# Kernel tuning notes

Measured on AMD Instinct MI355X. Metric: run time of the kernel, lower is better.

The kernel has to match this reference:

```python
import jax, jax.numpy as jnp
import numpy as np

N_GRAPHS = 128   # number of graphs in the batch
G = 128          # nodes per graph (equal-sized ragged blocks for the reference)
D = 512          # node embedding dim (feature_dim)
EPS = 1e-7


def setup_inputs() -> dict:
    key = jax.random.key(0)
    embeddings = jax.random.normal(key, (N_GRAPHS * G, D), dtype=jnp.float32)
    # Precompute block-diagonal strict-upper-triangular mask as gather indices.
    # Equivalent to torch.block_diag(*[triu(ones(g,g), diagonal=1) for g in sizes]).bool()
    iu_r, iu_c = np.triu_indices(G, k=1)                 # per-block triu(.,1) indices
    offsets = (np.arange(N_GRAPHS) * G)[:, None]         # block offsets into [N, N]
    row_idx = jnp.asarray((offsets + iu_r[None, :]).ravel(), dtype=jnp.int32)
    col_idx = jnp.asarray((offsets + iu_c[None, :]).ravel(), dtype=jnp.int32)
    return {"embeddings": embeddings, "row_idx": row_idx, "col_idx": col_idx}


def reference(embeddings, row_idx, col_idx):
    # Full NxN dot-product similarity (N = total nodes across all graphs).
    sims = embeddings @ embeddings.T                     # [N, N]
    m = sims.min()
    M = sims.max()
    sims = (sims - m) / (M - m + EPS)                    # global min-max normalization
    # Gather block-diagonal strict-upper-triangular entries -> flat vector.
    return sims[row_idx, col_idx]                        # [sum_g g*(g-1)/2]
```

## Files before the change

kernel.cpp:

```cpp
#include <hip/hip_runtime.h>
#include <hip/hip_bf16.h>
#include <stdint.h>


typedef __attribute__((ext_vector_type(8))) __bf16 bf16x8;
typedef __attribute__((ext_vector_type(16))) float floatx16;
typedef __attribute__((ext_vector_type(4))) int intx4;
typedef __attribute__((ext_vector_type(16))) int intx16;

#define AS1 __attribute__((address_space(1)))
#define AS3 __attribute__((address_space(3)))

static constexpr int DIM      = 512;
static constexpr int NTILE    = 128;
static constexpr int GX       = 72;
static constexpr int NPAIRIDX = 65 * 128;
static constexpr float QS     = 19.5f;
static constexpr int MARGIN_I = 3042;


static __device__ __forceinline__ unsigned short f2bf_rne(float f) {
  unsigned int u = __float_as_uint(f);
  u += 0x7fffu + ((u >> 16) & 1u);
  return (unsigned short)(u >> 16);
}
static __device__ __forceinline__ int fkey(float f) {
  int s = __float_as_int(f);
  return s >= 0 ? s : (s ^ 0x7fffffff);
}
static __device__ __forceinline__ float funkey(int k) {
  return __int_as_float(k >= 0 ? k : (k ^ 0x7fffffff));
}
static __device__ __forceinline__ int swzd(int row, int c16) {
  return c16 ^ (row & 15);
}
static __device__ __forceinline__ int swz8(int row, int c8) {
  return c8 ^ (row & 7);
}
static __device__ __forceinline__ int qswap(int v) {
  return (v & 0x7A) | ((v & 1) << 2) | ((v >> 2) & 1);
}
static __device__ __forceinline__ int sfun(int row) {
  return (row & 3) ^ ((row >> 3) & 3);
}

__global__ void k_convert(const float* __restrict__ in,
                          unsigned short* __restrict__ bf,
                          char* __restrict__ q,
                          int* __restrict__ ctrl, int n4) {
  int i = blockIdx.x * blockDim.x + threadIdx.x;
  if (i == 0) {
    ctrl[0] = 0x7fffffff; ctrl[1] = (int)0x80000000;
    ctrl[2] = 0x7fffffff;
  }
  if (i >= n4) return;
  float4 v = ((const float4*)in)[i];
  ushort4 o;
  o.x = f2bf_rne(v.x); o.y = f2bf_rne(v.y);
  o.z = f2bf_rne(v.z); o.w = f2bf_rne(v.w);
  ((ushort4*)bf)[i] = o;
  int qx = __float2int_rn(v.x * QS), qy = __float2int_rn(v.y * QS);
  int qz = __float2int_rn(v.z * QS), qw = __float2int_rn(v.w * QS);
  char4 c;
  c.x = (char)min(127, max(-127, qx));
  c.y = (char)min(127, max(-127, qy));
  c.z = (char)min(127, max(-127, qz));
  c.w = (char)min(127, max(-127, qw));
  ((char4*)q)[i] = c;
}

__global__ __launch_bounds__(512, 4) void k_gemm(
    const char* __restrict__ Eq,
    const unsigned short* __restrict__ E,
    int* __restrict__ ipart,
    float* __restrict__ diagblocks,
    int* __restrict__ ctrl) {
  const int x  = blockIdx.x;
  const int tr = blockIdx.y;
  if (x > 64) return;
  const int pi = tr * 65 + x;

  const int tid = threadIdx.x;
  __shared__ __align__(16) char smem[2][24576];
  __shared__ float2 redbuf[8];
  __shared__ int iredbuf[8];

  const int w = tid >> 6, lane = tid & 63;
  const int l31 = lane & 31;
  const int kg  = lane >> 5;

  if (x < 64) {
    const int tc1 = 2 * x + 1;
    if (tc1 <= tr) {
      if (tid == 0) ipart[pi] = 0x7fffffff;
      return;
    }
    const int tc0 = (2 * x > tr) ? 2 * x : tc1;

    const int rowA  = tr  * 128;
    const int rowB0 = tc0 * 128;
    const int rowB1 = tc1 * 128;

    const int wr = w >> 2;
    const int wcq = w & 3;
    const int bplane = 8192 + (wcq >> 1) * 8192;

    intx16 acc[2][2];
#pragma unroll
    for (int i = 0; i < 2; i++)
#pragma unroll
      for (int j = 0; j < 2; j++)
#pragma unroll
        for (int r = 0; r < 16; r++) acc[i][j][r] = 0;

#define STAGE3(bb, kt) do {                                                   \
    int p_   = tid;                                                           \
    int q_   = p_ >> 2;                                                       \
    int row_ = qswap(q_);                                                     \
    int off_ = (kt) * 64 + (((p_ & 3) ^ sfun(row_)) * 16);                    \
    char* d_ = smem[bb] + p_ * 16;                                            \
    __builtin_amdgcn_global_load_lds(                                         \
        (const AS1 unsigned int*)(Eq + (size_t)(rowA + row_) * DIM + off_),   \
        (AS3 unsigned int*)d_, 16, 0, 0);                                     \
    __builtin_amdgcn_global_load_lds(                                         \
        (const AS1 unsigned int*)(Eq + (size_t)(rowB0 + row_) * DIM + off_),  \
        (AS3 unsigned int*)(d_ + 8192), 16, 0, 0);                            \
    __builtin_amdgcn_global_load_lds(                                         \
        (const AS1 unsigned int*)(Eq + (size_t)(rowB1 + row_) * DIM + off_),  \
        (AS3 unsigned int*)(d_ + 16384), 16, 0, 0);                           \
  } while (0)

    const int ra0 = wr * 64 + l31,        ra1 = wr * 64 + 32 + l31;
    const int rb0 = (wcq & 1) * 64 + l31, rb1 = (wcq & 1) * 64 + 32 + l31;
    const int pa0 = qswap(ra0) * 64, sa0 = sfun(ra0);
    const int pa1 = qswap(ra1) * 64, sa1 = sfun(ra1);
    const int pb0 = qswap(rb0) * 64, sb0 = sfun(rb0);
    const int pb1 = qswap(rb1) * 64, sb1 = sfun(rb1);

    STAGE3(0, 0);
    __syncthreads();

#pragma unroll
    for (int kt = 0; kt < 8; kt++) {
      if (kt + 1 < 8) STAGE3((kt + 1) & 1, kt + 1);
      const char* cb = smem[kt & 1];
#pragma unroll
      for (int ks = 0; ks < 2; ks++) {
        const int c = ks * 2 + kg;
        intx4 af0 = *(const intx4*)(cb +           pa0 + ((c ^ sa0) << 4));
        intx4 af1 = *(const intx4*)(cb +           pa1 + ((c ^ sa1) << 4));
        intx4 bf0 = *(const intx4*)(cb + bplane +  pb0 + ((c ^ sb0) << 4));
        intx4 bf1 = *(const intx4*)(cb + bplane +  pb1 + ((c ^ sb1) << 4));
        acc[0][0] = __builtin_amdgcn_mfma_i32_32x32x32_i8(af0, bf0, acc[0][0], 0, 0, 0);
        acc[0][1] = __builtin_amdgcn_mfma_i32_32x32x32_i8(af0, bf1, acc[0][1], 0, 0, 0);
        acc[1][0] = __builtin_amdgcn_mfma_i32_32x32x32_i8(af1, bf0, acc[1][0], 0, 0, 0);
        acc[1][1] = __builtin_amdgcn_mfma_i32_32x32x32_i8(af1, bf1, acc[1][1], 0, 0, 0);
      }
      __syncthreads();
    }
#undef STAGE3

    int vmin = 0x7fffffff;
#pragma unroll
    for (int ti = 0; ti < 2; ti++)
#pragma unroll
      for (int tj = 0; tj < 2; tj++)
#pragma unroll
        for (int r = 0; r < 16; r++) vmin = min(vmin, acc[ti][tj][r]);
#pragma unroll
    for (int m_ = 32; m_ >= 1; m_ >>= 1)
      vmin = min(vmin, __shfl_xor(vmin, m_));
    if (lane == 0) iredbuf[w] = vmin;
    __syncthreads();
    if (tid == 0) {
      int mn = iredbuf[0];
      for (int i = 1; i < 8; i++) mn = min(mn, iredbuf[i]);
      ipart[pi] = mn;
      atomicMin(&ctrl[2], mn);
    }
  } else {
    if (tid == 0) ipart[pi] = 0x7fffffff;
    unsigned short* lA = (unsigned short*)&smem[0][0];
    const int wr = w >> 2, wcq = w & 3;
    floatx16 acc[2];
#pragma unroll
    for (int t = 0; t < 2; t++)
#pragma unroll
      for (int r = 0; r < 16; r++) acc[t][r] = 0.f;

    const int rowBase = tr * 128;

    for (int kb = 0; kb < 4; kb++) {
      const int kBase = kb * 128;
#pragma unroll
      for (int j = 0; j < 4; j++) {
        int p   = j * 512 + tid;
        int row = p >> 4, c16 = p & 15;
        int sc = swzd(row, c16);
        const unsigned short* gA =
            E + (size_t)(rowBase + row) * DIM + kBase + sc * 8;
        __builtin_amdgcn_global_load_lds((const AS1 unsigned int*)gA,
                                         (AS3 unsigned int*)(lA + p * 8), 16, 0, 0);
      }
      __syncthreads();

#pragma unroll
      for (int ks = 0; ks < 8; ks++) {
        bf16x8 af[2], bfv;
        const int c16 = ks * 2 + kg;
#pragma unroll
        for (int t = 0; t < 2; t++) {
          int ra = wr * 64 + t * 32 + l31;
          af[t]  = *(const bf16x8*)(lA + ra * 128 + swzd(ra, c16) * 8);
        }
        {
          int rb = wcq * 32 + l31;
          bfv = *(const bf16x8*)(lA + rb * 128 + swzd(rb, c16) * 8);
        }
#pragma unroll
        for (int t = 0; t < 2; t++)
          acc[t] = __builtin_amdgcn_mfma_f32_32x32x16_bf16(
              af[t], bfv, acc[t], 0, 0, 0);
      }
      __syncthreads();
    }

    float vmin = 3.4e38f, vmax = -3.4e38f;
#pragma unroll
    for (int t = 0; t < 2; t++)
#pragma unroll
      for (int r = 0; r < 16; r++) {
        float v = acc[t][r];
        vmin = fminf(vmin, v);
        vmax = fmaxf(vmax, v);
      }
#pragma unroll
    for (int m_ = 32; m_ >= 1; m_ >>= 1) {
      vmin = fminf(vmin, __shfl_xor(vmin, m_));
      vmax = fmaxf(vmax, __shfl_xor(vmax, m_));
    }
    if (lane == 0) redbuf[w] = make_float2(vmin, vmax);
    __syncthreads();
    if (tid == 0) {
      float mn = redbuf[0].x, mx = redbuf[0].y;
      for (int i = 1; i < 8; i++) {
        mn = fminf(mn, redbuf[i].x);
        mx = fmaxf(mx, redbuf[i].y);
      }
      atomicMin(&ctrl[0], fkey(mn));
      atomicMax(&ctrl[1], fkey(mx));
    }

    float* Bout = diagblocks + (size_t)tr * (128 * 128);
    const int cbase = wcq * 32 + l31;
#pragma unroll
    for (int t = 0; t < 2; t++) {
#pragma unroll
      for (int r = 0; r < 16; r++) {
        int row = wr * 64 + t * 32 + (r & 3) + 8 * (r >> 2) + 4 * kg;
        Bout[row * 128 + cbase] = acc[t][r];
      }
    }
  }
}

__global__ __launch_bounds__(256) void k_refine(
    const unsigned short* __restrict__ E,
    const int* __restrict__ ipart, int* __restrict__ ctrl) {
  const int pi = blockIdx.x;
  if (ipart[pi] > ctrl[2] + MARGIN_I) return;
  const int tr = pi / 65, x = pi % 65;
  if (x == 64) return;

  const int tid = threadIdx.x;
  __shared__ __align__(16) unsigned short lA[128 * 64];
  __shared__ __align__(16) unsigned short lB[128 * 64];
  __shared__ float redbuf[4];

  const int w = tid >> 6, lane = tid & 63;
  const int wr = w >> 1, wc = w & 1;
  const int l31 = lane & 31;
  const int kg  = lane >> 5;

  for (int s = 0; s < 2; s++) {
    const int tc = 2 * x + s;
    if (tc <= tr) continue;

    floatx16 acc[2][2];
#pragma unroll
    for (int i = 0; i < 2; i++)
#pragma unroll
      for (int j = 0; j < 2; j++)
#pragma unroll
        for (int r = 0; r < 16; r++) acc[i][j][r] = 0.f;

    const int rowBaseA = tr * 128;
    const int rowBaseB = tc * 128;

    for (int kb = 0; kb < 8; kb++) {
      const int kBase = kb * 64;
#pragma unroll
      for (int j = 0; j < 4; j++) {
        int cb  = (w * 4 + j) * 64;
        int p   = cb + lane;
        int row = p >> 3, c8 = p & 7;
        int sc8 = swz8(row, c8);
        const unsigned short* gA = E + (size_t)(rowBaseA + row) * DIM + kBase + sc8 * 8;
        const unsigned short* gB = E + (size_t)(rowBaseB + row) * DIM + kBase + sc8 * 8;
        __builtin_amdgcn_global_load_lds((const AS1 unsigned int*)gA,
                                         (AS3 unsigned int*)(lA + cb * 8), 16, 0, 0);
        __builtin_amdgcn_global_load_lds((const AS1 unsigned int*)gB,
                                         (AS3 unsigned int*)(lB + cb * 8), 16, 0, 0);
      }
      __syncthreads();

#pragma unroll
      for (int ks = 0; ks < 4; ks++) {
        bf16x8 af[2], bfv[2];
        const int c8 = ks * 2 + kg;
#pragma unroll
        for (int t = 0; t < 2; t++) {
          int ra = wr * 64 + t * 32 + l31;
          int rb = wc * 64 + t * 32 + l31;
          af[t]  = *(const bf16x8*)(lA + (ra * 8 + swz8(ra, c8)) * 8);
          bfv[t] = *(const bf16x8*)(lB + (rb * 8 + swz8(rb, c8)) * 8);
        }
#pragma unroll
        for (int ti = 0; ti < 2; ti++)
#pragma unroll
          for (int tj = 0; tj < 2; tj++)
            acc[ti][tj] = __builtin_amdgcn_mfma_f32_32x32x16_bf16(
                af[ti], bfv[tj], acc[ti][tj], 0, 0, 0);
      }
      __syncthreads();
    }

    float vmin = 3.4e38f;
#pragma unroll
    for (int ti = 0; ti < 2; ti++)
#pragma unroll
      for (int tj = 0; tj < 2; tj++)
#pragma unroll
        for (int r = 0; r < 16; r++) vmin = fminf(vmin, acc[ti][tj][r]);
#pragma unroll
    for (int m_ = 32; m_ >= 1; m_ >>= 1)
      vmin = fminf(vmin, __shfl_xor(vmin, m_));
    if (lane == 0) redbuf[w] = vmin;
    __syncthreads();
    if (tid == 0) {
      float mn = redbuf[0];
      for (int i = 1; i < 4; i++) mn = fminf(mn, redbuf[i]);
      atomicMin(&ctrl[0], fkey(mn));
    }
    __syncthreads();
  }
}

__global__ __launch_bounds__(256) void k_gather(
    const int* __restrict__ rix, const int* __restrict__ cix,
    const float* __restrict__ blocks, const int* __restrict__ ctrl,
    float* __restrict__ out, int n) {
  int i = blockIdx.x * blockDim.x + threadIdx.x;
  if (i >= n) return;
  float m   = funkey(ctrl[0]);
  float M   = funkey(ctrl[1]);
  float inv = 1.0f / (M - m + 1e-7f);
  int r = rix[i], c = cix[i];
  int g = r >> 7;
  float v = blocks[((size_t)g << 14) + ((r & 127) << 7) + (c & 127)];
  out[i] = (v - m) * inv;
}

extern "C" void kernel_launch(void* const* d_in, const int* in_sizes, int n_in,
                              void* d_out, int out_size, void* d_ws, size_t ws_size,
                              hipStream_t stream) {
  const float* emb = (const float*)d_in[0];
  const int* rix   = (const int*)d_in[1];
  const int* cix   = (const int*)d_in[2];

  char* ws = (char*)d_ws;
  int* ctrl           = (int*)ws;
  unsigned short* Ebf = (unsigned short*)(ws + 256);
  char* Eq            = (char*)(ws + 256 + (16u << 20));
  float* diagblocks   = (float*)(ws + 256 + (24u << 20));
  int* ipart          = (int*)(ws + 256 + (32u << 20));

  int n4 = in_sizes[0] / 4;

  k_convert<<<(n4 + 255) / 256, 256, 0, stream>>>(emb, Ebf, Eq, ctrl, n4);

  k_gemm<<<dim3(GX, 128), 512, 0, stream>>>(Eq, Ebf, ipart, diagblocks, ctrl);

  k_refine<<<NPAIRIDX, 256, 0, stream>>>(Ebf, ipart, ctrl);

  k_gather<<<(out_size + 255) / 256, 256, 0, stream>>>(rix, cix, diagblocks,
                                                       ctrl, (float*)d_out,
                                                       out_size);
}
```

Before: 191.4 us.

## Use 256x256 int8 GEMM tiles with cyclic tile-pair scheduling for min search

Enlarges the int8 min-search GEMM tile from 128x256 to 256x256 per workgroup. The upper-triangular pair enumeration becomes a cyclic (y + x) mod 64 schedule, which gives each workgroup the same amount of work. The refine kernel and the diagonal-block work are remapped to the new slot layout. The aim is better operand reuse per LDS load and no wasted or idle blocks from the triangular mask, at the cost of doubled LDS, more accumulator registers and lower occupancy. Since 33 cyclic offsets cover some tile pairs twice, it also does some redundant compute.

```diff
diff --git a/kernel.cpp b/kernel.cpp
--- a/kernel.cpp
+++ b/kernel.cpp
@@ -12,9 +12,8 @@
 #define AS3 __attribute__((address_space(3)))
 
 static constexpr int DIM      = 512;
-static constexpr int NTILE    = 128;
-static constexpr int GX       = 72;
-static constexpr int NPAIRIDX = 65 * 128;
+static constexpr int SLOTX    = 40;
+static constexpr int NSLOT    = SLOTX * 64;
 static constexpr float QS     = 19.5f;
 static constexpr int MARGIN_I = 3042;
 
@@ -69,19 +68,19 @@
   ((char4*)q)[i] = c;
 }
 
-__global__ __launch_bounds__(512, 4) void k_gemm(
+__global__ __launch_bounds__(512, 2) void k_gemm(
     const char* __restrict__ Eq,
     const unsigned short* __restrict__ E,
     int* __restrict__ ipart,
     float* __restrict__ diagblocks,
     int* __restrict__ ctrl) {
-  const int x  = blockIdx.x;
-  const int tr = blockIdx.y;
-  if (x > 64) return;
-  const int pi = tr * 65 + x;
+  const int x = blockIdx.x;
+  const int y = blockIdx.y;
+  if (x > 34) return;
+  const int pi = y * SLOTX + x;
 
   const int tid = threadIdx.x;
-  __shared__ __align__(16) char smem[2][24576];
+  __shared__ __align__(16) char smem[2][32768];
   __shared__ float2 redbuf[8];
   __shared__ int iredbuf[8];
 
@@ -89,82 +88,85 @@
   const int l31 = lane & 31;
   const int kg  = lane >> 5;
 
-  if (x < 64) {
-    const int tc1 = 2 * x + 1;
-    if (tc1 <= tr) {
-      if (tid == 0) ipart[pi] = 0x7fffffff;
-      return;
-    }
-    const int tc0 = (2 * x > tr) ? 2 * x : tc1;
-
-    const int rowA  = tr  * 128;
-    const int rowB0 = tc0 * 128;
-    const int rowB1 = tc1 * 128;
-
-    const int wr = w >> 2;
-    const int wcq = w & 3;
-    const int bplane = 8192 + (wcq >> 1) * 8192;
-
-    intx16 acc[2][2];
+  if (x < 33) {
+    const int tt = (y + x) & 63;
+    const int rA0 = 256 * y,  rA1 = 256 * y + 128;
+    const int rB0 = 256 * tt, rB1 = 256 * tt + 128;
+
+    const int wr = w >> 1, wc = w & 1;
+
+    intx16 acc[2][4];
 #pragma unroll
     for (int i = 0; i < 2; i++)
 #pragma unroll
-      for (int j = 0; j < 2; j++)
+      for (int j = 0; j < 4; j++)
 #pragma unroll
         for (int r = 0; r < 16; r++) acc[i][j][r] = 0;
 
-#define STAGE3(bb, kt) do {                                                   \
-    int p_   = tid;                                                           \
-    int q_   = p_ >> 2;                                                       \
+#define STAGE4(bb, kt) do {                                                   \
+    int q_   = tid >> 2;                                                      \
     int row_ = qswap(q_);                                                     \
-    int off_ = (kt) * 64 + (((p_ & 3) ^ sfun(row_)) * 16);                    \
-    char* d_ = smem[bb] + p_ * 16;                                            \
+    int off_ = (kt) * 64 + (((tid & 3) ^ sfun(row_)) * 16);                   \
+    char* d_ = smem[bb] + tid * 16;                                           \
     __builtin_amdgcn_global_load_lds(                                         \
-        (const AS1 unsigned int*)(Eq + (size_t)(rowA + row_) * DIM + off_),   \
+        (const AS1 unsigned int*)(Eq + (size_t)(rA0 + row_) * DIM + off_),    \
         (AS3 unsigned int*)d_, 16, 0, 0);                                     \
     __builtin_amdgcn_global_load_lds(                                         \
-        (const AS1 unsigned int*)(Eq + (size_t)(rowB0 + row_) * DIM + off_),  \
+        (const AS1 unsigned int*)(Eq + (size_t)(rA1 + row_) * DIM + off_),    \
         (AS3 unsigned int*)(d_ + 8192), 16, 0, 0);                            \
     __builtin_amdgcn_global_load_lds(                                         \
-        (const AS1 unsigned int*)(Eq + (size_t)(rowB1 + row_) * DIM + off_),  \
+        (const AS1 unsigned int*)(Eq + (size_t)(rB0 + row_) * DIM + off_),    \
         (AS3 unsigned int*)(d_ + 16384), 16, 0, 0);                           \
+    __builtin_amdgcn_global_load_lds(                                         \
+        (const AS1 unsigned int*)(Eq + (size_t)(rB1 + row_) * DIM + off_),    \
+        (AS3 unsigned int*)(d_ + 24576), 16, 0, 0);                           \
   } while (0)
 
-    const int ra0 = wr * 64 + l31,        ra1 = wr * 64 + 32 + l31;
-    const int rb0 = (wcq & 1) * 64 + l31, rb1 = (wcq & 1) * 64 + 32 + l31;
-    const int pa0 = qswap(ra0) * 64, sa0 = sfun(ra0);
-    const int pa1 = qswap(ra1) * 64, sa1 = sfun(ra1);
-    const int pb0 = qswap(rb0) * 64, sb0 = sfun(rb0);
-    const int pb1 = qswap(rb1) * 64, sb1 = sfun(rb1);
-
-    STAGE3(0, 0);
+    const int ra0 = wr * 64 + l31, ra1 = wr * 64 + 32 + l31;
+    const int pa0 = (ra0 >> 7) * 8192 + qswap(ra0 & 127) * 64, sa0 = sfun(ra0 & 127);
+    const int pa1 = (ra1 >> 7) * 8192 + qswap(ra1 & 127) * 64, sa1 = sfun(ra1 & 127);
+    const int rb0 = 0 * 32 + l31, rb1 = 1 * 32 + l31;
+    const int rb2 = 2 * 32 + l31, rb3 = 3 * 32 + l31;
+    const int pbB = 16384 + wc * 8192;
+    const int pb0 = pbB + qswap(rb0) * 64, sb0 = sfun(rb0);
+    const int pb1 = pbB + qswap(rb1) * 64, sb1 = sfun(rb1);
+    const int pb2 = pbB + qswap(rb2) * 64, sb2 = sfun(rb2);
+    const int pb3 = pbB + qswap(rb3) * 64, sb3 = sfun(rb3);
+
+    STAGE4(0, 0);
     __syncthreads();
 
 #pragma unroll
     for (int kt = 0; kt < 8; kt++) {
-      if (kt + 1 < 8) STAGE3((kt + 1) & 1, kt + 1);
+      if (kt + 1 < 8) STAGE4((kt + 1) & 1, kt + 1);
       const char* cb = smem[kt & 1];
 #pragma unroll
       for (int ks = 0; ks < 2; ks++) {
         const int c = ks * 2 + kg;
-        intx4 af0 = *(const intx4*)(cb +           pa0 + ((c ^ sa0) << 4));
-        intx4 af1 = *(const intx4*)(cb +           pa1 + ((c ^ sa1) << 4));
-        intx4 bf0 = *(const intx4*)(cb + bplane +  pb0 + ((c ^ sb0) << 4));
-        intx4 bf1 = *(const intx4*)(cb + bplane +  pb1 + ((c ^ sb1) << 4));
-        acc[0][0] = __builtin_amdgcn_mfma_i32_32x32x32_i8(af0, bf0, acc[0][0], 0, 0, 0);
-        acc[0][1] = __builtin_amdgcn_mfma_i32_32x32x32_i8(af0, bf1, acc[0][1], 0, 0, 0);
-        acc[1][0] = __builtin_amdgcn_mfma_i32_32x32x32_i8(af1, bf0, acc[1][0], 0, 0, 0);
-        acc[1][1] = __builtin_amdgcn_mfma_i32_32x32x32_i8(af1, bf1, acc[1][1], 0, 0, 0);
-      }
-      __syncthreads();
-    }
-#undef STAGE3
+        intx4 af0 = *(const intx4*)(cb + pa0 + ((c ^ sa0) << 4));
+        intx4 af1 = *(const intx4*)(cb + pa1 + ((c ^ sa1) << 4));
+        intx4 b0  = *(const intx4*)(cb + pb0 + ((c ^ sb0) << 4));
+        intx4 b1  = *(const intx4*)(cb + pb1 + ((c ^ sb1) << 4));
+        intx4 b2  = *(const intx4*)(cb + pb2 + ((c ^ sb2) << 4));
+        intx4 b3  = *(const intx4*)(cb + pb3 + ((c ^ sb3) << 4));
+        acc[0][0] = __builtin_amdgcn_mfma_i32_32x32x32_i8(af0, b0, acc[0][0], 0, 0, 0);
+        acc[0][1] = __builtin_amdgcn_mfma_i32_32x32x32_i8(af0, b1, acc[0][1], 0, 0, 0);
+        acc[0][2] = __builtin_amdgcn_mfma_i32_32x32x32_i8(af0, b2, acc[0][2], 0, 0, 0);
+        acc[0][3] = __builtin_amdgcn_mfma_i32_32x32x32_i8(af0, b3, acc[0][3], 0, 0, 0);
+        acc[1][0] = __builtin_amdgcn_mfma_i32_32x32x32_i8(af1, b0, acc[1][0], 0, 0, 0);
+        acc[1][1] = __builtin_amdgcn_mfma_i32_32x32x32_i8(af1, b1, acc[1][1], 0, 0, 0);
+        acc[1][2] = __builtin_amdgcn_mfma_i32_32x32x32_i8(af1, b2, acc[1][2], 0, 0, 0);
+        acc[1][3] = __builtin_amdgcn_mfma_i32_32x32x32_i8(af1, b3, acc[1][3], 0, 0, 0);
+      }
+      __syncthreads();
+    }
+#undef STAGE4
 
     int vmin = 0x7fffffff;
 #pragma unroll
     for (int ti = 0; ti < 2; ti++)
 #pragma unroll
-      for (int tj = 0; tj < 2; tj++)
+      for (int tj = 0; tj < 4; tj++)
 #pragma unroll
         for (int r = 0; r < 16; r++) vmin = min(vmin, acc[ti][tj][r]);
 #pragma unroll
@@ -180,6 +182,7 @@
     }
   } else {
     if (tid == 0) ipart[pi] = 0x7fffffff;
+    const int tr = 2 * y + (x - 33);
     unsigned short* lA = (unsigned short*)&smem[0][0];
     const int wr = w >> 2, wcq = w & 3;
     floatx16 acc[2];
@@ -269,8 +272,9 @@
     const int* __restrict__ ipart, int* __restrict__ ctrl) {
   const int pi = blockIdx.x;
   if (ipart[pi] > ctrl[2] + MARGIN_I) return;
-  const int tr = pi / 65, x = pi % 65;
-  if (x == 64) return;
+  const int y = pi / SLOTX, x = pi % SLOTX;
+  if (x >= 33) return;
+  const int tt = (y + x) & 63;
 
   const int tid = threadIdx.x;
   __shared__ __align__(16) unsigned short lA[128 * 64];
@@ -282,9 +286,9 @@
   const int l31 = lane & 31;
   const int kg  = lane >> 5;
 
-  for (int s = 0; s < 2; s++) {
-    const int tc = 2 * x + s;
-    if (tc <= tr) continue;
+  for (int ab = 0; ab < 4; ab++) {
+    const int rowBaseA = (2 * y + (ab >> 1)) * 128;
+    const int rowBaseB = (2 * tt + (ab & 1)) * 128;
 
     floatx16 acc[2][2];
 #pragma unroll
@@ -293,9 +297,6 @@
       for (int j = 0; j < 2; j++)
 #pragma unroll
         for (int r = 0; r < 16; r++) acc[i][j][r] = 0.f;
-
-    const int rowBaseA = tr * 128;
-    const int rowBaseB = tc * 128;
 
     for (int kb = 0; kb < 8; kb++) {
       const int kBase = kb * 64;
@@ -384,14 +385,13 @@
   char* Eq            = (char*)(ws + 256 + (16u << 20));
   float* diagblocks   = (float*)(ws + 256 + (24u << 20));
   int* ipart          = (int*)(ws + 256 + (32u << 20));
-
   int n4 = in_sizes[0] / 4;
 
   k_convert<<<(n4 + 255) / 256, 256, 0, stream>>>(emb, Ebf, Eq, ctrl, n4);
 
-  k_gemm<<<dim3(GX, 128), 512, 0, stream>>>(Eq, Ebf, ipart, diagblocks, ctrl);
-
-  k_refine<<<NPAIRIDX, 256, 0, stream>>>(Ebf, ipart, ctrl);
+  k_gemm<<<dim3(SLOTX, 64), 512, 0, stream>>>(Eq, Ebf, ipart, diagblocks, ctrl);
+
+  k_refine<<<NSLOT, 256, 0, stream>>>(Ebf, ipart, ctrl);
 
   k_gather<<<(out_size + 255) / 256, 256, 0, stream>>>(rix, cix, diagblocks,
                                                        ctrl, (float*)d_out,
```

After: 200.1 us. +4.6%, slower.
